# Kernel optimization log

Measured on AMD Instinct MI355X. Metric: run time of the kernel, lower is better.

Reference implementation:

```python
import jax, jax.numpy as jnp
import numpy as np

N, D, H, DF = 2048, 1024, 16, 4096
DK = D // H
EPS = 1e-5


def layernorm(x, g, b):
    mu = jnp.mean(x, axis=-1, keepdims=True)
    var = jnp.mean((x - mu) ** 2, axis=-1, keepdims=True)
    return (x - mu) * jax.lax.rsqrt(var + EPS) * g + b


def setup_inputs() -> dict:
    key = jax.random.key(0)
    ks = jax.random.split(key, 8)
    s = 0.02
    return {
        "X": jax.random.normal(ks[0], (N, D), dtype=jnp.float32),
        "Wqkv": jax.random.normal(ks[1], (2 * D, D), dtype=jnp.float32) * s,
        "W1": jax.random.normal(ks[2], (DF, D), dtype=jnp.float32) * s,
        "b1": jnp.zeros((DF,), dtype=jnp.float32),
        "W2": jax.random.normal(ks[3], (D, DF), dtype=jnp.float32) * s,
        "b2": jnp.zeros((D,), dtype=jnp.float32),
        "g1": jnp.ones((D,), dtype=jnp.float32),
        "be1": jnp.zeros((D,), dtype=jnp.float32),
        "g2": jnp.ones((D,), dtype=jnp.float32),
        "be2": jnp.zeros((D,), dtype=jnp.float32),
    }


def reference(X, Wqkv, W1, b1, W2, b2, g1, be1, g2, be2):
    # shared-QK multi-head attention (Q == K), no bias
    qkv = X @ Wqkv.T                      # [N, 2D]
    qk, v = jnp.split(qkv, 2, axis=-1)    # [N, D] each
    qk = qk.reshape(N, H, DK)
    v = v.reshape(N, H, DK)
    scale = DK ** 0.5
    scores = jnp.einsum('nhd,mhd->hnm', qk, qk) / scale  # [H, N, N]
    att = jax.nn.softmax(scores, axis=-1)
    attn_out = jnp.einsum('hnm,mhd->nhd', att, v).reshape(N, D)
    # residual + LN, FFN (dropout is identity in eval), residual + LN
    h = layernorm(X + attn_out, g1, be1)
    ffn = jax.nn.relu(h @ W1.T + b1) @ W2.T + b2
    return layernorm(h + ffn, g2, be2)
```

## Files before the change

kernel.cpp:

```cpp
#include <hip/hip_runtime.h>
#include <stdint.h>


#define NTOK 2048
#define DMODEL 1024
#define NHEAD 16
#define DHEAD 64
#define DFF 4096

typedef __attribute__((ext_vector_type(8))) short short8;
typedef __attribute__((ext_vector_type(4))) short short4v;
typedef __attribute__((ext_vector_type(4))) float f32x4;

__device__ __forceinline__ float fexp2(float x) { return __builtin_amdgcn_exp2f(x); }

__device__ __forceinline__ short f2b(float f) {
  union { float f; unsigned u; } v; v.f = f;
  unsigned r = v.u + 0x7fffu + ((v.u >> 16) & 1u);
  return (short)(r >> 16);
}

__device__ __forceinline__ void gload_lds16(const void* g, void* l) {
  __builtin_amdgcn_global_load_lds((const __attribute__((address_space(1))) void*)g,
                                   (__attribute__((address_space(3))) void*)l,
                                   16, 0, 0);
}

__global__ void cast_all(const float* __restrict__ s0, short* __restrict__ d0, int n0,
                         const float* __restrict__ s1, short* __restrict__ d1, int n1,
                         const float* __restrict__ s2, short* __restrict__ d2, int n2,
                         const float* __restrict__ s3, short* __restrict__ d3, int n3) {
  int i = blockIdx.x * blockDim.x + threadIdx.x;
  const float* s; short* d; int j = i;
  if (j < n0) { s = s0; d = d0; }
  else { j -= n0;
    if (j < n1) { s = s1; d = d1; }
    else { j -= n1;
      if (j < n2) { s = s2; d = d2; }
      else { j -= n2; if (j >= n3) return; s = s3; d = d3; }
    }
  }
  const float4* p = (const float4*)(s + (size_t)j * 8);
  float4 a = p[0], b = p[1];
  short8 o;
  o[0] = f2b(a.x); o[1] = f2b(a.y); o[2] = f2b(a.z); o[3] = f2b(a.w);
  o[4] = f2b(b.x); o[5] = f2b(b.y); o[6] = f2b(b.z); o[7] = f2b(b.w);
  *(short8*)(d + (size_t)j * 8) = o;
}

template<int BM, int BN, int WR, int WC, bool BF16OUT, bool BIAS, bool RELU>
__launch_bounds__(WR * WC * 64)
__global__ void gemm_bt(const short* __restrict__ A, const short* __restrict__ B,
                        const float* __restrict__ bias,
                        float* __restrict__ Cf, short* __restrict__ Cb,
                        int M, int N, int K, int lda, int ldb, int kstep) {
  constexpr int BK = 32;
  constexpr int THREADS = WR * WC * 64;
  constexpr int AISS = (BM * BK) / (8 * THREADS);
  constexpr int BISS = (BN * BK) / (8 * THREADS);
  __shared__ short As[BM * BK];
  __shared__ short Bs[BN * BK];
  const int t = threadIdx.x;
  const int l = t & 63;
  const int w = t >> 6;
  const int wr = w / WC, wc = w % WC;
  const int lr = l & 15, lg = l >> 4;
  const int m0 = blockIdx.y * BM, n0 = blockIdx.x * BN;
  const int koff = blockIdx.z * kstep;
  A += koff; B += koff;
  Cf += (size_t)blockIdx.z * M * N;
  f32x4 acc[4][4] = {};
  for (int k0 = 0; k0 < K; k0 += BK) {
#pragma unroll
    for (int i = 0; i < AISS; ++i) {
      int e = (i * THREADS + t) * 8;
      int r = e >> 5, c = e & 31;
      gload_lds16(A + (size_t)(m0 + r) * lda + k0 + c, As + (size_t)(i * THREADS + w * 64) * 8);
    }
#pragma unroll
    for (int i = 0; i < BISS; ++i) {
      int e = (i * THREADS + t) * 8;
      int r = e >> 5, c = e & 31;
      gload_lds16(B + (size_t)(n0 + r) * ldb + k0 + c, Bs + (size_t)(i * THREADS + w * 64) * 8);
    }
    __syncthreads();
    short8 a[4], b[4];
#pragma unroll
    for (int m = 0; m < 4; ++m)
      a[m] = *(const short8*)(As + (wr * 64 + m * 16 + lr) * BK + lg * 8);
#pragma unroll
    for (int n = 0; n < 4; ++n)
      b[n] = *(const short8*)(Bs + (wc * 64 + n * 16 + lr) * BK + lg * 8);
#pragma unroll
    for (int m = 0; m < 4; ++m)
#pragma unroll
      for (int n = 0; n < 4; ++n)
        acc[m][n] = __builtin_amdgcn_mfma_f32_16x16x32_bf16(a[m], b[n], acc[m][n], 0, 0, 0);
    __syncthreads();
  }
#pragma unroll
  for (int n = 0; n < 4; ++n) {
    const int col = n0 + wc * 64 + n * 16 + lr;
    const float bv = BIAS ? bias[col] : 0.0f;
#pragma unroll
    for (int m = 0; m < 4; ++m) {
#pragma unroll
      for (int r = 0; r < 4; ++r) {
        const int row = m0 + wr * 64 + m * 16 + lg * 4 + r;
        float v = acc[m][n][r] + bv;
        if (RELU) v = fmaxf(v, 0.0f);
        if (BF16OUT) Cb[(size_t)row * N + col] = f2b(v);
        else         Cf[(size_t)row * N + col] = v;
      }
    }
  }
}

__global__ void transpose_v(const short* __restrict__ src, short* __restrict__ dst) {
  __shared__ short tile[64][65];
  const int bx = blockIdx.x * 64;
  const int by = blockIdx.y * 64;
  const int t = threadIdx.x;
  const int tx = t & 63, ty = t >> 6;
#pragma unroll
  for (int i = 0; i < 64; i += 4)
    tile[ty + i][tx] = src[(size_t)(by + ty + i) * 2048 + 1024 + bx + tx];
  __syncthreads();
#pragma unroll
  for (int i = 0; i < 64; i += 4)
    dst[(size_t)(bx + ty + i) * 2048 + by + tx] = tile[tx][ty + i];
}

__launch_bounds__(256, 2)
__global__ void flash_attn(const short* __restrict__ qk, const short* __restrict__ vt,
                           float* __restrict__ O) {
  const int t = threadIdx.x;
  const int l = t & 63, w = t >> 6;
  const int lr = l & 15, lg = l >> 4;
  const int h = blockIdx.y;
  const int qb = blockIdx.x;
  __shared__ short Ks[2][64 * 64];
  __shared__ short Vs[2][64 * 64];
  __shared__ short Pl[4][16][72];
  const float C2 = 0.18033688011112042f;

  const int qrow = qb * 64 + w * 16 + lr;
  short8 aq[2];
#pragma unroll
  for (int f = 0; f < 2; ++f)
    aq[f] = *(const short8*)(qk + (size_t)qrow * 2048 + h * 64 + f * 32 + lg * 8);

  f32x4 o[4] = {};
  float mrun = -1e30f, lrun = 0.0f;

  auto stage = [&](int b, int kt) {
#pragma unroll
    for (int i = 0; i < 2; ++i) {
      const int chunk = i * 256 + w * 64 + l;
      const int r = chunk >> 3, c = chunk & 7;
      const int cs = c ^ (r & 7);
      gload_lds16(qk + (size_t)(kt * 64 + r) * 2048 + h * 64 + cs * 8,
                  &Ks[b][(size_t)(i * 256 + w * 64) * 8]);
    }
#pragma unroll
    for (int i = 0; i < 2; ++i) {
      const int chunk = i * 256 + w * 64 + l;
      const int r = chunk >> 3, c = chunk & 7;
      const int cs = c ^ (r & 7);
      gload_lds16(vt + (size_t)(h * 64 + r) * 2048 + kt * 64 + cs * 8,
                  &Vs[b][(size_t)(i * 256 + w * 64) * 8]);
    }
  };

  stage(0, 0);
  __syncthreads();

#pragma unroll 1
  for (int kt = 0; kt < 32; ++kt) {
    const int cur = kt & 1;
    if (kt + 1 < 32) stage(cur ^ 1, kt + 1);

    f32x4 s[4] = {};
#pragma unroll
    for (int f = 0; f < 2; ++f) {
      short8 kf[4];
#pragma unroll
      for (int n = 0; n < 4; ++n) {
        const int r = n * 16 + lr;
        kf[n] = *(const short8*)(&Ks[cur][r * 64 + (((f * 4 + lg) ^ (lr & 7)) * 8)]);
      }
#pragma unroll
      for (int n = 0; n < 4; ++n)
        s[n] = __builtin_amdgcn_mfma_f32_16x16x32_bf16(kf[n], aq[f], s[n], 0, 0, 0);
    }
    float m0 = fmaxf(fmaxf(s[0][0], s[0][1]), fmaxf(s[0][2], s[0][3]));
    float m1 = fmaxf(fmaxf(s[1][0], s[1][1]), fmaxf(s[1][2], s[1][3]));
    float m2 = fmaxf(fmaxf(s[2][0], s[2][1]), fmaxf(s[2][2], s[2][3]));
    float m3 = fmaxf(fmaxf(s[3][0], s[3][1]), fmaxf(s[3][2], s[3][3]));
    float tm = fmaxf(fmaxf(m0, m1), fmaxf(m2, m3));
    tm = fmaxf(tm, __shfl_xor(tm, 16));
    tm = fmaxf(tm, __shfl_xor(tm, 32));
    const float mnew = fmaxf(mrun, tm);
    const float corr = fexp2((mrun - mnew) * C2);
    mrun = mnew;
    float p[4][4];
#pragma unroll
    for (int n = 0; n < 4; ++n)
#pragma unroll
      for (int r = 0; r < 4; ++r)
        p[n][r] = fexp2((s[n][r] - mnew) * C2);
    float q0 = (p[0][0] + p[0][1]) + (p[0][2] + p[0][3]);
    float q1 = (p[1][0] + p[1][1]) + (p[1][2] + p[1][3]);
    float q2 = (p[2][0] + p[2][1]) + (p[2][2] + p[2][3]);
    float q3 = (p[3][0] + p[3][1]) + (p[3][2] + p[3][3]);
    float ps = (q0 + q1) + (q2 + q3);
    ps += __shfl_xor(ps, 16);
    ps += __shfl_xor(ps, 32);
    lrun = lrun * corr + ps;
    f32x4 cov;
#pragma unroll
    for (int r = 0; r < 4; ++r)
      cov[r] = __shfl(corr, lg * 4 + r);
#pragma unroll
    for (int n = 0; n < 4; ++n)
      o[n] *= cov;
#pragma unroll
    for (int n = 0; n < 4; ++n) {
      uint2 wv;
      wv.x = ((unsigned)(unsigned short)f2b(p[n][1]) << 16) | (unsigned short)f2b(p[n][0]);
      wv.y = ((unsigned)(unsigned short)f2b(p[n][3]) << 16) | (unsigned short)f2b(p[n][2]);
      *(uint2*)&Pl[w][lr][n * 16 + lg * 4] = wv;
    }
#pragma unroll
    for (int f = 0; f < 2; ++f) {
      short8 ap = *(const short8*)&Pl[w][lr][f * 32 + lg * 8];
      short8 vf[4];
#pragma unroll
      for (int n = 0; n < 4; ++n) {
        const int r = n * 16 + lr;
        vf[n] = *(const short8*)(&Vs[cur][r * 64 + (((f * 4 + lg) ^ (lr & 7)) * 8)]);
      }
#pragma unroll
      for (int n = 0; n < 4; ++n)
        o[n] = __builtin_amdgcn_mfma_f32_16x16x32_bf16(ap, vf[n], o[n], 0, 0, 0);
    }
    __syncthreads();
  }

  f32x4 inv;
#pragma unroll
  for (int r = 0; r < 4; ++r)
    inv[r] = 1.0f / __shfl(lrun, lg * 4 + r);
#pragma unroll
  for (int n = 0; n < 4; ++n)
#pragma unroll
    for (int r = 0; r < 4; ++r)
      O[(size_t)(qb * 64 + w * 16 + lg * 4 + r) * 1024 + h * 64 + n * 16 + lr] = o[n][r] * inv[r];
}

__launch_bounds__(256)
__global__ void add_ln(const float* __restrict__ A, const float* __restrict__ B0,
                       const float* __restrict__ B1, const float* __restrict__ bias,
                       const float* __restrict__ g, const float* __restrict__ be,
                       float* __restrict__ outf, short* __restrict__ outb) {
  const int row = blockIdx.x;
  const int t = threadIdx.x;
  const size_t base = (size_t)row * 1024 + t * 4;
  float4 a = *(const float4*)(A + base);
  float4 b = *(const float4*)(B0 + base);
  float4 s; s.x = a.x + b.x; s.y = a.y + b.y; s.z = a.z + b.z; s.w = a.w + b.w;
  if (B1) {
    float4 c = *(const float4*)(B1 + base);
    s.x += c.x; s.y += c.y; s.z += c.z; s.w += c.w;
  }
  if (bias) {
    float4 c = *(const float4*)(bias + t * 4);
    s.x += c.x; s.y += c.y; s.z += c.z; s.w += c.w;
  }
  float sum = s.x + s.y + s.z + s.w;
  float sq  = s.x * s.x + s.y * s.y + s.z * s.z + s.w * s.w;
#pragma unroll
  for (int d = 32; d > 0; d >>= 1) {
    sum += __shfl_down(sum, d);
    sq  += __shfl_down(sq, d);
  }
  __shared__ float red[8];
  const int w = t >> 6, l = t & 63;
  if (l == 0) { red[w] = sum; red[4 + w] = sq; }
  __syncthreads();
  sum = red[0] + red[1] + red[2] + red[3];
  sq  = red[4] + red[5] + red[6] + red[7];
  const float mu = sum * (1.0f / 1024.0f);
  const float rstd = rsqrtf(sq * (1.0f / 1024.0f) - mu * mu + 1e-5f);
  float4 gv = *(const float4*)(g + t * 4);
  float4 bv = *(const float4*)(be + t * 4);
  float4 o;
  o.x = (s.x - mu) * rstd * gv.x + bv.x;
  o.y = (s.y - mu) * rstd * gv.y + bv.y;
  o.z = (s.z - mu) * rstd * gv.z + bv.z;
  o.w = (s.w - mu) * rstd * gv.w + bv.w;
  *(float4*)(outf + base) = o;
  if (outb) {
    short4v ob; ob.x = f2b(o.x); ob.y = f2b(o.y); ob.z = f2b(o.z); ob.w = f2b(o.w);
    *(short4v*)(outb + base) = ob;
  }
}

extern "C" void kernel_launch(void* const* d_in, const int* in_sizes, int n_in,
                              void* d_out, int out_size, void* d_ws, size_t ws_size,
                              hipStream_t stream) {
  const float* X    = (const float*)d_in[0];
  const float* Wqkv = (const float*)d_in[1];
  const float* W1   = (const float*)d_in[2];
  const float* b1   = (const float*)d_in[3];
  const float* W2   = (const float*)d_in[4];
  const float* b2   = (const float*)d_in[5];
  const float* g1   = (const float*)d_in[6];
  const float* be1  = (const float*)d_in[7];
  const float* g2   = (const float*)d_in[8];
  const float* be2  = (const float*)d_in[9];

  char* ws = (char*)d_ws;
  const size_t MiB = 1u << 20;
  short*  W1b   = (short*)(ws + 0 * MiB);
  short*  W2b   = (short*)(ws + 8 * MiB);
  short*  qkvb  = (short*)(ws + 16 * MiB);
  short*  vt    = (short*)(ws + 24 * MiB);
  short*  Xb    = (short*)(ws + 28 * MiB);
  short*  Wqkvb = (short*)(ws + 32 * MiB);
  float*  attn  = (float*)(ws + 36 * MiB);
  float*  h     = (float*)(ws + 44 * MiB);
  short*  hb    = (short*)(ws + 52 * MiB);
  short*  y1b   = (short*)(ws + 16 * MiB);
  float*  P0    = (float*)(ws + 52 * MiB);
  float*  P1    = P0 + (size_t)NTOK * DMODEL;

  cast_all<<<6144, 256, 0, stream>>>(X, Xb, NTOK * DMODEL / 8,
                                     Wqkv, Wqkvb, 2 * DMODEL * DMODEL / 8,
                                     W1, W1b, DFF * DMODEL / 8,
                                     W2, W2b, DMODEL * DFF / 8);

  {
    dim3 grid(2 * DMODEL / 128, NTOK / 128, 1);
    gemm_bt<128, 128, 2, 2, true, false, false><<<grid, 256, 0, stream>>>(
        Xb, Wqkvb, nullptr, nullptr, qkvb, NTOK, 2 * DMODEL, DMODEL, DMODEL, DMODEL, 0);
  }
  {
    dim3 grid(DMODEL / 64, NTOK / 64);
    transpose_v<<<grid, 256, 0, stream>>>(qkvb, vt);
  }
  {
    dim3 grid(NTOK / 64, NHEAD);
    flash_attn<<<grid, 256, 0, stream>>>(qkvb, vt, attn);
  }
  add_ln<<<NTOK, 256, 0, stream>>>(X, attn, nullptr, nullptr, g1, be1, h, hb);
  {
    dim3 grid(DFF / 128, NTOK / 128, 1);
    gemm_bt<128, 128, 2, 2, true, true, true><<<grid, 256, 0, stream>>>(
        hb, W1b, b1, nullptr, y1b, NTOK, DFF, DMODEL, DMODEL, DMODEL, 0);
  }
  {
    dim3 grid(DMODEL / 128, NTOK / 128, 2);
    gemm_bt<128, 128, 2, 2, false, false, false><<<grid, 256, 0, stream>>>(
        y1b, W2b, nullptr, P0, nullptr, NTOK, DMODEL, 2048, DFF, DFF, 2048);
  }
  add_ln<<<NTOK, 256, 0, stream>>>(h, P0, P1, b2, g2, be2, (float*)d_out, nullptr);
}
```

Baseline: 277.0 us.

## Double-buffer GEMM LDS tiles with BK=64 and XOR-swizzled layout

The shared GEMM kernel now uses a K tile of 64, two LDS buffers so the next tile's global-to-LDS load is issued while the current tile is consumed by MFMAs, and an XOR swizzle on the 16-byte chunk index to avoid LDS bank conflicts on fragment reads. This halves the number of barriers per K and overlaps memory with compute. The workspace layout is reshuffled so buffers don't alias under the new usage. LDS use quadruples per block, which may lower occupancy.

```diff
diff --git a/kernel.cpp b/kernel.cpp
--- a/kernel.cpp
+++ b/kernel.cpp
@@ -54,12 +54,12 @@
                         const float* __restrict__ bias,
                         float* __restrict__ Cf, short* __restrict__ Cb,
                         int M, int N, int K, int lda, int ldb, int kstep) {
-  constexpr int BK = 32;
+  constexpr int BK = 64;
   constexpr int THREADS = WR * WC * 64;
-  constexpr int AISS = (BM * BK) / (8 * THREADS);
-  constexpr int BISS = (BN * BK) / (8 * THREADS);
-  __shared__ short As[BM * BK];
-  __shared__ short Bs[BN * BK];
+  constexpr int ACH = (BM * (BK / 8)) / THREADS;
+  constexpr int BCH = (BN * (BK / 8)) / THREADS;
+  __shared__ short As[2][BM * BK];
+  __shared__ short Bs[2][BN * BK];
   const int t = threadIdx.x;
   const int l = t & 63;
   const int w = t >> 6;
@@ -69,33 +69,52 @@
   const int koff = blockIdx.z * kstep;
   A += koff; B += koff;
   Cf += (size_t)blockIdx.z * M * N;
+
+  auto stage = [&](int b, int k0) {
+#pragma unroll
+    for (int i = 0; i < ACH; ++i) {
+      const int ci = i * THREADS + t;
+      const int r = ci >> 3, c = ci & 7;
+      const int cs = c ^ (r & 7);
+      gload_lds16(A + (size_t)(m0 + r) * lda + k0 + cs * 8,
+                  &As[b][(size_t)(i * THREADS + w * 64) * 8]);
+    }
+#pragma unroll
+    for (int i = 0; i < BCH; ++i) {
+      const int ci = i * THREADS + t;
+      const int r = ci >> 3, c = ci & 7;
+      const int cs = c ^ (r & 7);
+      gload_lds16(B + (size_t)(n0 + r) * ldb + k0 + cs * 8,
+                  &Bs[b][(size_t)(i * THREADS + w * 64) * 8]);
+    }
+  };
+
   f32x4 acc[4][4] = {};
-  for (int k0 = 0; k0 < K; k0 += BK) {
-#pragma unroll
-    for (int i = 0; i < AISS; ++i) {
-      int e = (i * THREADS + t) * 8;
-      int r = e >> 5, c = e & 31;
-      gload_lds16(A + (size_t)(m0 + r) * lda + k0 + c, As + (size_t)(i * THREADS + w * 64) * 8);
-    }
-#pragma unroll
-    for (int i = 0; i < BISS; ++i) {
-      int e = (i * THREADS + t) * 8;
-      int r = e >> 5, c = e & 31;
-      gload_lds16(B + (size_t)(n0 + r) * ldb + k0 + c, Bs + (size_t)(i * THREADS + w * 64) * 8);
-    }
-    __syncthreads();
-    short8 a[4], b[4];
-#pragma unroll
-    for (int m = 0; m < 4; ++m)
-      a[m] = *(const short8*)(As + (wr * 64 + m * 16 + lr) * BK + lg * 8);
-#pragma unroll
-    for (int n = 0; n < 4; ++n)
-      b[n] = *(const short8*)(Bs + (wc * 64 + n * 16 + lr) * BK + lg * 8);
-#pragma unroll
-    for (int m = 0; m < 4; ++m)
-#pragma unroll
-      for (int n = 0; n < 4; ++n)
-        acc[m][n] = __builtin_amdgcn_mfma_f32_16x16x32_bf16(a[m], b[n], acc[m][n], 0, 0, 0);
+  const int nIter = K / BK;
+  stage(0, 0);
+  __syncthreads();
+  for (int it = 0; it < nIter; ++it) {
+    const int cur = it & 1;
+    if (it + 1 < nIter) stage(cur ^ 1, (it + 1) * BK);
+#pragma unroll
+    for (int kk = 0; kk < 2; ++kk) {
+      short8 a[4], b[4];
+#pragma unroll
+      for (int m = 0; m < 4; ++m) {
+        const int r = wr * 64 + m * 16 + lr;
+        a[m] = *(const short8*)(&As[cur][r * BK + (((kk * 4 + lg) ^ (r & 7)) * 8)]);
+      }
+#pragma unroll
+      for (int n = 0; n < 4; ++n) {
+        const int r = wc * 64 + n * 16 + lr;
+        b[n] = *(const short8*)(&Bs[cur][r * BK + (((kk * 4 + lg) ^ (r & 7)) * 8)]);
+      }
+#pragma unroll
+      for (int m = 0; m < 4; ++m)
+#pragma unroll
+        for (int n = 0; n < 4; ++n)
+          acc[m][n] = __builtin_amdgcn_mfma_f32_16x16x32_bf16(a[m], b[n], acc[m][n], 0, 0, 0);
+    }
     __syncthreads();
   }
 #pragma unroll
@@ -324,16 +343,16 @@
   const size_t MiB = 1u << 20;
   short*  W1b   = (short*)(ws + 0 * MiB);
   short*  W2b   = (short*)(ws + 8 * MiB);
-  short*  qkvb  = (short*)(ws + 16 * MiB);
-  short*  vt    = (short*)(ws + 24 * MiB);
-  short*  Xb    = (short*)(ws + 28 * MiB);
-  short*  Wqkvb = (short*)(ws + 32 * MiB);
-  float*  attn  = (float*)(ws + 36 * MiB);
-  float*  h     = (float*)(ws + 44 * MiB);
-  short*  hb    = (short*)(ws + 52 * MiB);
-  short*  y1b   = (short*)(ws + 16 * MiB);
-  float*  P0    = (float*)(ws + 52 * MiB);
+  float*  h     = (float*)(ws + 16 * MiB);
+  short*  hb    = (short*)(ws + 24 * MiB);
+  short*  qkvb  = (short*)(ws + 28 * MiB);
+  short*  y1b   = (short*)(ws + 28 * MiB);
+  short*  vt    = (short*)(ws + 36 * MiB);
+  float*  attn  = (float*)(ws + 44 * MiB);
+  float*  P0    = (float*)(ws + 44 * MiB);
   float*  P1    = P0 + (size_t)NTOK * DMODEL;
+  short*  Xb    = (short*)(ws + 52 * MiB);
+  short*  Wqkvb = (short*)(ws + 56 * MiB);
 
   cast_all<<<6144, 256, 0, stream>>>(X, Xb, NTOK * DMODEL / 8,
                                      Wqkv, Wqkvb, 2 * DMODEL * DMODEL / 8,
```

New measurement: 251.1 us. 9.3% less time.
